# Optimization experiments

Measured on AMD Instinct MI355X. Metric: run time of the kernel, lower is better.

## Reference

```python
import jax, jax.numpy as jnp
import numpy as np

N_JOBS, N_MACH = 30, 20
N = N_JOBS * N_MACH          # 600 nodes
IN_DIM = 2
H = 128                      # hidden_dim_feature_extractor
HA = 256                     # hidden_dim_actor
HC = 256                     # hidden_dim_critic
E = 9600                     # edges
BN_EPS = 1e-5


def setup_inputs() -> dict:
    key = jax.random.key(0)
    ks = jax.random.split(key, 16)
    init = lambda k, shp: (jax.random.normal(k, shp, jnp.float32) * 0.05)
    d = {
        "features": jax.random.normal(ks[0], (N, IN_DIM), jnp.float32),
        "edge_index": jax.random.randint(ks[1], (2, E), 0, N, jnp.int32),
        # GIN layer 0 MLP: Linear(IN,H) -> BN -> ReLU -> Linear(H,H)
        "g0_W0": init(ks[2], (IN_DIM, H)), "g0_b0": jnp.zeros((H,), jnp.float32),
        "g0_gamma": jnp.ones((H,), jnp.float32), "g0_beta": jnp.zeros((H,), jnp.float32),
        "g0_W1": init(ks[3], (H, H)), "g0_b1": jnp.zeros((H,), jnp.float32),
        # GIN layer 1 MLP: Linear(H,H) -> BN -> ReLU -> Linear(H,H)
        "g1_W0": init(ks[4], (H, H)), "g1_b0": jnp.zeros((H,), jnp.float32),
        "g1_gamma": jnp.ones((H,), jnp.float32), "g1_beta": jnp.zeros((H,), jnp.float32),
        "g1_W1": init(ks[5], (H, H)), "g1_b1": jnp.zeros((H,), jnp.float32),
        # actor MLP: Linear(3H,HA) -> ReLU -> Linear(HA,1)
        "a_W0": init(ks[6], (3 * H, HA)), "a_b0": jnp.zeros((HA,), jnp.float32),
        "a_W1": init(ks[7], (HA, 1)), "a_b1": jnp.zeros((1,), jnp.float32),
        # critic MLP: Linear(H,HC) -> ReLU -> Linear(HC,1)
        "c_W0": init(ks[8], (H, HC)), "c_b0": jnp.zeros((HC,), jnp.float32),
        "c_W1": init(ks[9], (HC, 1)), "c_b1": jnp.zeros((1,), jnp.float32),
    }
    return d


def _gin_mlp(h, W0, b0, gamma, beta, W1, b1):
    # Linear -> BatchNorm(train-mode batch stats) -> ReLU -> Linear
    h1 = h @ W0 + b0
    mu = h1.mean(axis=0)
    var = h1.var(axis=0)
    h1 = gamma * (h1 - mu) * jax.lax.rsqrt(var + BN_EPS) + beta
    return jax.nn.relu(h1) @ W1 + b1


def reference(features, edge_index,
              g0_W0, g0_b0, g0_gamma, g0_beta, g0_W1, g0_b1,
              g1_W0, g1_b0, g1_gamma, g1_beta, g1_W1, g1_b1,
              a_W0, a_b0, a_W1, a_b1,
              c_W0, c_b0, c_W1, c_b1):
    src, dst = edge_index[0], edge_index[1]

    def gin(x, *mlp_params):
        # GINConv with eps=0: MLP(x + sum_{j in N(i)} x_j)
        agg = jax.ops.segment_sum(x[src], dst, num_segments=N)
        return _gin_mlp(x + agg, *mlp_params)

    h = gin(features, g0_W0, g0_b0, g0_gamma, g0_beta, g0_W1, g0_b1)
    h = gin(h, g1_W0, g1_b0, g1_gamma, g1_beta, g1_W1, g1_b1)   # (N, H)

    # graph pooling: (ones/N) @ h  == mean over nodes
    ge = h.mean(axis=0, keepdims=True)                           # (1, H)
    value = jax.nn.relu(ge @ c_W0 + c_b0) @ c_W1 + c_b1          # (1, 1)

    # s_a_pairs row k (k = i*N + j): [ge, h[j] (tile), h[i] (repeat_interleave)]
    # Fuse concat + first actor matmul by splitting a_W0 into three H-blocks.
    Ws, Wn1, Wn2 = a_W0[:H], a_W0[H:2 * H], a_W0[2 * H:]
    pre = (ge @ Ws + a_b0)[None, :, :] + (h @ Wn1)[None, :, :] + (h @ Wn2)[:, None, :]
    logits = jax.nn.relu(pre).reshape(N * N, HA) @ a_W1 + a_b1   # (N^2, 1)
    pi = jax.nn.softmax(logits, axis=0)
    return pi, value
```

## Files before the change

kernel.cpp:

```cpp
#include <hip/hip_runtime.h>
#include <math.h>

#define N_NODES 600
#define N_EDGES 9600
#define HDIM    128
#define HA      256
#define HC      256
#define NN      360000
#define BN_EPS  1e-5f
#define NTILE   361

#define OFF_U      0
#define OFF_BCONST 1200
#define OFF_BF     1456
#define OFF_SUMZ   1584
#define OFF_SUMZ2  1712
#define OFF_R1SUM  1840
#define OFF_RACC   1968
#define OFF_SUMA   2736
#define OFF_CSR    3248
#define OFF_WF     13456
#define OFF_WC1    29840
#define OFF_WC2    62608
#define OFF_WGS    95376
#define OFF_Z      128144
#define OFF_A      204944
#define OFF_B      358544

typedef _Float16 h2 __attribute__((ext_vector_type(2)));
typedef _Float16 h4 __attribute__((ext_vector_type(4)));
typedef _Float16 h8 __attribute__((ext_vector_type(8)));

__device__ __forceinline__ float dot2acc(h2 a, h2 b, float c) {
#if __has_builtin(__builtin_amdgcn_fdot2)
  return __builtin_amdgcn_fdot2(a, b, c, false);
#else
  return c + (float)a.x * (float)b.x + (float)a.y * (float)b.y;
#endif
}

__device__ __forceinline__ h2 relu2(h2 x) {
  h2 z = {(_Float16)0, (_Float16)0};
#if __has_builtin(__builtin_elementwise_max)
  return __builtin_elementwise_max(x, z);
#else
  h2 r;
  r.x = x.x > z.x ? x.x : z.x;
  r.y = x.y > z.y ? x.y : z.y;
  return r;
#endif
}

__device__ __forceinline__ h4 toh4(float4 v) {
  h4 r;
  r.x = (_Float16)v.x; r.y = (_Float16)v.y;
  r.z = (_Float16)v.z; r.w = (_Float16)v.w;
  return r;
}

struct KP {
  const float* feat; const int* ei;
  const float *g0W0, *g0ga, *g0be, *g0W1, *g0b1;
  const float *g1W0, *g1ga, *g1be, *g1W1, *g1b1;
  const float *aW0, *ab0, *aW1;
  const float *cW0, *cb0, *cW1, *cb1;
  float* ws; float* out;
};

__global__ __launch_bounds__(256) void k_indep(KP p) {
  __shared__ float sm[1536];
  const int b = blockIdx.x, t = threadIdx.x;

  if (b < 25) {
    float* us = sm;
    if (t < 48) us[t] = 0.f;
    __syncthreads();
    const int lo = b * 24, hi = lo + 24;
    for (int e = t; e < N_EDGES; e += 256) {
      int d = p.ei[N_EDGES + e];
      if (d >= lo && d < hi) {
        int s = p.ei[e];
        atomicAdd(&us[2 * (d - lo)],     p.feat[2 * s]);
        atomicAdd(&us[2 * (d - lo) + 1], p.feat[2 * s + 1]);
      }
    }
    __syncthreads();
    if (t < 48) p.ws[OFF_U + b * 48 + t] = us[t] + p.feat[b * 48 + t];
  } else if (b == 25) {
    int* si = (int*)sm;
    int* cnt = si; int* bs = si + 600; int* off = si + 856;
    int* rs_g = (int*)(p.ws + OFF_CSR);
    int* src_g = rs_g + 604;
    for (int i = t; i < 600; i += 256) cnt[i] = 0;
    __syncthreads();
    for (int e = t; e < N_EDGES; e += 256) atomicAdd(&cnt[p.ei[N_EDGES + e]], 1);
    __syncthreads();
    int lsum = 0;
    if (t < 200) lsum = cnt[3 * t] + cnt[3 * t + 1] + cnt[3 * t + 2];
    bs[t] = lsum; __syncthreads();
    for (int d = 1; d < 256; d <<= 1) {
      int v = (t >= d) ? bs[t - d] : 0;
      __syncthreads();
      bs[t] += v;
      __syncthreads();
    }
    if (t < 200) {
      int base = bs[t] - lsum;
      off[3 * t] = base;
      off[3 * t + 1] = base + cnt[3 * t];
      off[3 * t + 2] = base + cnt[3 * t] + cnt[3 * t + 1];
    }
    if (t == 0) off[600] = N_EDGES;
    __syncthreads();
    for (int i = t; i < 601; i += 256) rs_g[i] = off[i];
    for (int i = t; i < 600; i += 256) cnt[i] = off[i];
    __syncthreads();
    for (int e = t; e < N_EDGES; e += 256) {
      int d = p.ei[N_EDGES + e];
      int pos = atomicAdd(&cnt[d], 1);
      src_g[pos] = p.ei[e];
    }
  } else if (b < 42) {
    int o = (b - 26) * 1024 + t * 4;
    int j = o >> 7, c = o & 127;
    float4 acc = make_float4(0, 0, 0, 0);
#pragma unroll 8
    for (int m = 0; m < HDIM; m++) {
      float w = p.g0W1[j * HDIM + m];
      const float4 v = *(const float4*)(p.g1W0 + m * HDIM + c);
      acc.x += w * v.x; acc.y += w * v.y; acc.z += w * v.z; acc.w += w * v.w;
    }
    *(float4*)(p.ws + OFF_WF + j * HDIM + c) = acc;
  } else {
    p.ws[OFF_RACC + t] = 0.f;
    if (t < 128) {
      float a2 = 0.f;
#pragma unroll 8
      for (int m = 0; m < HDIM; m++) a2 += p.g0b1[m] * p.g1W0[m * HDIM + t];
      p.ws[OFF_BF + t] = a2;
      p.ws[OFF_SUMZ + t] = 0.f;
      p.ws[OFF_SUMZ2 + t] = 0.f;
      p.ws[OFF_R1SUM + t] = 0.f;
    }
  }
}

__global__ __launch_bounds__(256) void k_zagg(KP p) {
  __shared__ float2 u2[600];
  __shared__ float bn[384];
  __shared__ float r0agg[512];
  __shared__ float red[256];
  __shared__ float wred[24];
  const int b = blockIdx.x, t = threadIdx.x;

  if (b >= 150) {
    if (b < 246) {
      int o = (b - 150) * 1024 + t * 4;
      int mat = o >> 15, rem = o & 32767;
      int j = rem >> 8, k = rem & 255;
      int rowbase = (mat == 0) ? HDIM : (mat == 1 ? 2 * HDIM : 0);
      const float* aw = p.aW0 + rowbase * HA + k;
      float4 acc = make_float4(0, 0, 0, 0);
#pragma unroll 8
      for (int m = 0; m < HDIM; m++) {
        float w = p.g1W1[j * HDIM + m];
        const float4 v = *(const float4*)(aw + m * HA);
        acc.x += w * v.x; acc.y += w * v.y; acc.z += w * v.z; acc.w += w * v.w;
      }
      int dst = (mat == 0) ? OFF_WC1 : (mat == 1 ? OFF_WC2 : OFF_WGS);
      *(float4*)(p.ws + dst + j * HA + k) = acc;
    } else {
      float acc = 0.f;
#pragma unroll 8
      for (int m = 0; m < HDIM; m++) {
        float gb = p.g1b1[m];
        acc += gb * (p.aW0[m * HA + t] + p.aW0[(HDIM + m) * HA + t] +
                     p.aW0[(2 * HDIM + m) * HA + t]);
      }
      p.ws[OFF_BCONST + t] = p.ab0[t] + acc;
    }
    return;
  }

  const int n0 = b * 4;
  const float2* ug = (const float2*)(p.ws + OFF_U);
  for (int i = t; i < 600; i += 256) u2[i] = ug[i];
  __syncthreads();
  float s0 = 0, s1 = 0, s00 = 0, s11 = 0, s01 = 0;
  for (int n = t; n < N_NODES; n += 256) {
    float u0 = u2[n].x, u1 = u2[n].y;
    s0 += u0; s1 += u1; s00 += u0 * u0; s11 += u1 * u1; s01 += u0 * u1;
  }
#pragma unroll
  for (int off = 32; off > 0; off >>= 1) {
    s0  += __shfl_xor(s0, off);  s1  += __shfl_xor(s1, off);
    s00 += __shfl_xor(s00, off); s11 += __shfl_xor(s11, off);
    s01 += __shfl_xor(s01, off);
  }
  const int wv = t >> 6, ln = t & 63;
  if (ln == 0) {
    wred[wv * 5 + 0] = s0;  wred[wv * 5 + 1] = s1;  wred[wv * 5 + 2] = s00;
    wred[wv * 5 + 3] = s11; wred[wv * 5 + 4] = s01;
  }
  __syncthreads();
  if (t < HDIM) {
    float tot[5];
#pragma unroll
    for (int q = 0; q < 5; q++)
      tot[q] = wred[q] + wred[5 + q] + wred[10 + q] + wred[15 + q];
    float m0 = tot[0] / 600.f, m1 = tot[1] / 600.f;
    float v00 = tot[2] / 600.f - m0 * m0;
    float v11 = tot[3] / 600.f - m1 * m1;
    float v01 = tot[4] / 600.f - m0 * m1;
    float W00 = p.g0W0[t], W01 = p.g0W0[HDIM + t];
    float var = W00 * W00 * v00 + W01 * W01 * v11 + 2.f * W00 * W01 * v01;
    float sc = p.g0ga[t] * rsqrtf(var + BN_EPS);
    float mu = m0 * W00 + m1 * W01;
    bn[t] = sc * W00; bn[128 + t] = sc * W01; bn[256 + t] = p.g0be[t] - mu * sc;
  }
  __syncthreads();
  const int* rs = (const int*)(p.ws + OFF_CSR);
  const int* srcv = rs + 604;
#pragma unroll
  for (int pq = 0; pq < 2; pq++) {
    int idx = pq * 256 + t, n = idx >> 7, c = idx & 127, node = n0 + n;
    float b0c = bn[c], b1c = bn[128 + c], b2c = bn[256 + c];
    float2 uo = u2[node];
    float acc = fmaxf(uo.x * b0c + uo.y * b1c + b2c, 0.f);
    int e0 = rs[node], e1 = rs[node + 1];
    for (int e = e0; e < e1; e++) {
      float2 us = u2[srcv[e]];
      acc += fmaxf(us.x * b0c + us.y * b1c + b2c, 0.f);
    }
    r0agg[n * 128 + c] = acc;
  }
  __syncthreads();
  const float* Wf = p.ws + OFF_WF;
  const float* bf = p.ws + OFF_BF;
  float zs = 0.f, zs2 = 0.f;
#pragma unroll
  for (int pq = 0; pq < 2; pq++) {
    int idx = pq * 256 + t, n = idx >> 7, c = idx & 127, node = n0 + n;
    const float* row = r0agg + n * 128;
    int deg = rs[node + 1] - rs[node];
    float acc = (1.f + (float)deg) * bf[c];
#pragma unroll 8
    for (int j = 0; j < HDIM; j++) acc += row[j] * Wf[j * HDIM + c];
    p.ws[OFF_Z + node * HDIM + c] = acc;
    zs += acc; zs2 += acc * acc;
  }
  red[t] = zs; __syncthreads();
  if (t < 128) atomicAdd(&p.ws[OFF_SUMZ + t], red[t] + red[t + 128]);
  __syncthreads();
  red[t] = zs2; __syncthreads();
  if (t < 128) atomicAdd(&p.ws[OFF_SUMZ2 + t], red[t] + red[t + 128]);
}

__global__ __launch_bounds__(256) void k_rab(KP p) {
  __shared__ float r1[4 * 128];
  __shared__ float scl[128], shf[128], rsum4[128];
  const int b = blockIdx.x, t = threadIdx.x, n0 = b * 4;
  if (t < 128) {
    float mu = p.ws[OFF_SUMZ + t] * (1.f / 600.f);
    float var = p.ws[OFF_SUMZ2 + t] * (1.f / 600.f) - mu * mu;
    float sc = p.g1ga[t] * rsqrtf(var + BN_EPS);
    scl[t] = sc; shf[t] = p.g1be[t] - mu * sc;
  }
  __syncthreads();
#pragma unroll
  for (int pq = 0; pq < 2; pq++) {
    int idx = pq * 256 + t, n = idx >> 7, j = idx & 127;
    float z = p.ws[OFF_Z + (n0 + n) * HDIM + j];
    r1[n * 128 + j] = fmaxf(z * scl[j] + shf[j], 0.f);
  }
  __syncthreads();
  if (t < 128) {
    float s = r1[t] + r1[128 + t] + r1[256 + t] + r1[384 + t];
    rsum4[t] = s;
    atomicAdd(&p.ws[OFF_R1SUM + t], s);
  }
  __syncthreads();
  const float* wc1 = p.ws + OFF_WC1;
  const float* wc2 = p.ws + OFF_WC2;
  const float* wgs = p.ws + OFF_WGS;
  float a0 = 0, a1 = 0, a2 = 0, a3 = 0, b0 = 0, b1 = 0, b2 = 0, b3 = 0, rc = 0;
#pragma unroll 4
  for (int j = 0; j < HDIM; j++) {
    float w1 = wc1[j * HA + t], w2 = wc2[j * HA + t], wg = wgs[j * HA + t];
    float r0v = r1[j], r1v = r1[128 + j], r2v = r1[256 + j], r3v = r1[384 + j];
    a0 += r0v * w1; a1 += r1v * w1; a2 += r2v * w1; a3 += r3v * w1;
    b0 += r0v * w2; b1 += r1v * w2; b2 += r2v * w2; b3 += r3v * w2;
    rc += rsum4[j] * wg;
  }
  atomicAdd(&p.ws[OFF_RACC + t], rc);
  float* A = p.ws + OFF_A; float* Bm = p.ws + OFF_B;
  A[n0 * HA + t] = a0; A[(n0 + 1) * HA + t] = a1;
  A[(n0 + 2) * HA + t] = a2; A[(n0 + 3) * HA + t] = a3;
  Bm[n0 * HA + t] = b0; Bm[(n0 + 1) * HA + t] = b1;
  Bm[(n0 + 2) * HA + t] = b2; Bm[(n0 + 3) * HA + t] = b3;
}

__global__ __launch_bounds__(256) void k_heads(KP p) {
  __shared__ h4 AsL[2048];
  __shared__ h4 BsL[2048];
  __shared__ h4 wlp[64];
  __shared__ h4 hsp[64];
  __shared__ float hsl[256];
  __shared__ float ge[128];
  __shared__ float geh[128];
  __shared__ float red[256];
  const int b = blockIdx.x, t = threadIdx.x;

  hsl[t] = p.ws[OFF_RACC + t] * (1.f / 600.f) + p.ws[OFF_BCONST + t];

  if (b == 0) {
    if (t < 128) ge[t] = p.ws[OFF_R1SUM + t] * (1.f / 600.f);
    __syncthreads();
    if (t < 128) {
      float a0 = p.g1b1[t], a1 = 0.f, a2 = 0.f, a3 = 0.f;
#pragma unroll 4
      for (int j = 0; j < HDIM; j += 4) {
        a0 += ge[j]     * p.g1W1[(j)     * HDIM + t];
        a1 += ge[j + 1] * p.g1W1[(j + 1) * HDIM + t];
        a2 += ge[j + 2] * p.g1W1[(j + 2) * HDIM + t];
        a3 += ge[j + 3] * p.g1W1[(j + 3) * HDIM + t];
      }
      geh[t] = (a0 + a1) + (a2 + a3);
    }
    __syncthreads();
    {
      float v0 = p.cb0[t], v1 = 0.f, v2 = 0.f, v3 = 0.f;
#pragma unroll 4
      for (int c = 0; c < HDIM; c += 4) {
        v0 += geh[c]     * p.cW0[(c)     * HC + t];
        v1 += geh[c + 1] * p.cW0[(c + 1) * HC + t];
        v2 += geh[c + 2] * p.cW0[(c + 2) * HC + t];
        v3 += geh[c + 3] * p.cW0[(c + 3) * HC + t];
      }
      float v = fmaxf((v0 + v1) + (v2 + v3), 0.f);
      red[t] = v * p.cW1[t];
    }
    __syncthreads();
    for (int off = 128; off > 0; off >>= 1) {
      if (t < off) red[t] += red[t + off];
      __syncthreads();
    }
    if (t == 0) p.out[NN] = red[0] + p.cb1[0];
  }
  __syncthreads();
  if (t < 64) {
    wlp[t] = toh4(*(const float4*)(p.aW1 + 4 * t));
    hsp[t] = toh4(*(const float4*)(hsl + 4 * t));
  }
  __syncthreads();

  const int tj = b % 19, ti = b / 19;
  const int j0 = tj * 32, i0 = ti * 32;
  const float* A  = p.ws + OFF_A;
  const float* Bm = p.ws + OFF_B;
#pragma unroll
  for (int q = 0; q < 8; q++) {
    int f = q * 256 + t;
    int r = f >> 6;
    int c4 = f & 63;
    int k = c4 * 4;
    int sw = c4 * 32 + (r ^ (c4 & 30));
    float4 av = (j0 + r < N_NODES) ? *(const float4*)(A + (j0 + r) * HA + k)
                                   : make_float4(0, 0, 0, 0);
    AsL[sw] = toh4(av) + hsp[c4];
    float4 bv = (i0 + r < N_NODES) ? *(const float4*)(Bm + (i0 + r) * HA + k)
                                   : make_float4(0, 0, 0, 0);
    BsL[sw] = toh4(bv);
  }
  __syncthreads();

  const int tx = t & 15, ty = t >> 4;
  const int jl = tx * 2, il = ty * 2;
  float a00 = 0, a01 = 0, a10 = 0, a11 = 0;
#pragma unroll 8
  for (int kk2 = 0; kk2 < 64; kk2++) {
    int s = kk2 & 30;
    h8 va = *(h8*)&AsL[kk2 * 32 + (jl ^ s)];
    h8 vb = *(h8*)&BsL[kk2 * 32 + (il ^ s)];
    h4 vw = wlp[kk2];
    h2 wlo = __builtin_shufflevector(vw, vw, 0, 1);
    h2 whi = __builtin_shufflevector(vw, vw, 2, 3);
    h2 aj0lo = __builtin_shufflevector(va, va, 0, 1);
    h2 aj0hi = __builtin_shufflevector(va, va, 2, 3);
    h2 aj1lo = __builtin_shufflevector(va, va, 4, 5);
    h2 aj1hi = __builtin_shufflevector(va, va, 6, 7);
    h2 bi0lo = __builtin_shufflevector(vb, vb, 0, 1);
    h2 bi0hi = __builtin_shufflevector(vb, vb, 2, 3);
    h2 bi1lo = __builtin_shufflevector(vb, vb, 4, 5);
    h2 bi1hi = __builtin_shufflevector(vb, vb, 6, 7);
    a00 = dot2acc(relu2(aj0lo + bi0lo), wlo, a00);
    a00 = dot2acc(relu2(aj0hi + bi0hi), whi, a00);
    a01 = dot2acc(relu2(aj1lo + bi0lo), wlo, a01);
    a01 = dot2acc(relu2(aj1hi + bi0hi), whi, a01);
    a10 = dot2acc(relu2(aj0lo + bi1lo), wlo, a10);
    a10 = dot2acc(relu2(aj0hi + bi1hi), whi, a10);
    a11 = dot2acc(relu2(aj1lo + bi1lo), wlo, a11);
    a11 = dot2acc(relu2(aj1hi + bi1hi), whi, a11);
  }

  const int gi = i0 + il, gj = j0 + jl;
  const bool vi0 = gi < N_NODES, vi1 = gi + 1 < N_NODES;
  const bool vj0 = gj < N_NODES, vj1 = gj + 1 < N_NODES;
  float s = 0.f;
  if (vi0 && vj0) { float e = __expf(a00); p.out[gi * N_NODES + gj] = e; s += e; }
  if (vi0 && vj1) { float e = __expf(a01); p.out[gi * N_NODES + gj + 1] = e; s += e; }
  if (vi1 && vj0) { float e = __expf(a10); p.out[(gi + 1) * N_NODES + gj] = e; s += e; }
  if (vi1 && vj1) { float e = __expf(a11); p.out[(gi + 1) * N_NODES + gj + 1] = e; s += e; }
  __syncthreads();
  red[t] = s;
  __syncthreads();
  for (int off = 128; off > 0; off >>= 1) {
    if (t < off) red[t] += red[t + off];
    __syncthreads();
  }
  if (t == 0) p.ws[OFF_SUMA + b] = red[0];
}

__global__ __launch_bounds__(256) void k_fin(KP p) {
  __shared__ float red[256];
  const int b = blockIdx.x, t = threadIdx.x;
  const float* suma = p.ws + OFF_SUMA;
  float s = (t < NTILE ? suma[t] : 0.f) + (t + 256 < NTILE ? suma[t + 256] : 0.f);
  red[t] = s;
  __syncthreads();
  for (int off = 128; off > 0; off >>= 1) {
    if (t < off) red[t] += red[t + off];
    __syncthreads();
  }
  const float inv = 1.0f / red[0];
#pragma unroll
  for (int pass = 0; pass < 3; pass++) {
    int f4 = pass * 256 + t;
    if (f4 < 600) {
      int r = f4 / 150, c4 = (f4 % 150) * 4;
      float* pp = p.out + (b * 4 + r) * N_NODES + c4;
      float4 v = *(const float4*)pp;
      v.x *= inv; v.y *= inv; v.z *= inv; v.w *= inv;
      *(float4*)pp = v;
    }
  }
}

extern "C" void kernel_launch(void* const* d_in, const int* in_sizes, int n_in,
                              void* d_out, int out_size, void* d_ws, size_t ws_size,
                              hipStream_t stream) {
  KP p;
  p.feat = (const float*)d_in[0];
  p.ei   = (const int*)  d_in[1];
  p.g0W0 = (const float*)d_in[2];
  p.g0ga = (const float*)d_in[4];  p.g0be = (const float*)d_in[5];
  p.g0W1 = (const float*)d_in[6];  p.g0b1 = (const float*)d_in[7];
  p.g1W0 = (const float*)d_in[8];
  p.g1ga = (const float*)d_in[10]; p.g1be = (const float*)d_in[11];
  p.g1W1 = (const float*)d_in[12]; p.g1b1 = (const float*)d_in[13];
  p.aW0  = (const float*)d_in[14]; p.ab0  = (const float*)d_in[15];
  p.aW1  = (const float*)d_in[16];
  p.cW0  = (const float*)d_in[18]; p.cb0  = (const float*)d_in[19];
  p.cW1  = (const float*)d_in[20]; p.cb1  = (const float*)d_in[21];
  p.ws   = (float*)d_ws;
  p.out  = (float*)d_out;

  k_indep<<<43,    256, 0, stream>>>(p);
  k_zagg <<<247,   256, 0, stream>>>(p);
  k_rab  <<<150,   256, 0, stream>>>(p);
  k_heads<<<NTILE, 256, 0, stream>>>(p);
  k_fin  <<<150,   256, 0, stream>>>(p);
}
```

Baseline: 78.41 us.

## Fuse five kernels into one persistent megakernel with atomic-counter stage gating

Replaces the five back-to-back kernel launches with a single kernel whose blocks are partitioned by stage. Blocks wait on global atomic arrival counters before consuming the previous stage's results, and a memset zeroes the counters and accumulators. The aim is to remove per-launch overhead and let independent precompute overlap with dependent stages. It relies on block dispatch order to avoid deadlock, since later-stage blocks spin while occupying CUs; all 951 blocks fit only if enough are resident, and the spin has a timeout break that could silently corrupt results.

After: 263.2 us. 236% more time.

```diff
diff --git a/kernel.cpp b/kernel.cpp
--- a/kernel.cpp
+++ b/kernel.cpp
@@ -10,22 +10,39 @@
 #define BN_EPS  1e-5f
 #define NTILE   361
 
-#define OFF_U      0
-#define OFF_BCONST 1200
-#define OFF_BF     1456
-#define OFF_SUMZ   1584
-#define OFF_SUMZ2  1712
-#define OFF_R1SUM  1840
-#define OFF_RACC   1968
-#define OFF_SUMA   2736
-#define OFF_CSR    3248
-#define OFF_WF     13456
-#define OFF_WC1    29840
-#define OFF_WC2    62608
-#define OFF_WGS    95376
-#define OFF_Z      128144
-#define OFF_A      204944
-#define OFF_B      358544
+#define B_PRE0   0
+#define B_CSR    25
+#define B_WF0    26
+#define B_BF     42
+#define B_WC0    43
+#define B_ZAGG0  140
+#define B_RAB0   290
+#define B_HEAD0  440
+#define B_FIN0   801
+#define NBLKS    951
+#define C1_TGT   43
+#define C2_TGT   247
+#define C3_TGT   150
+#define C4_TGT   361
+
+#define OFF_CNT    0
+#define OFF_SUMZ   16
+#define OFF_SUMZ2  144
+#define OFF_R1SUM  272
+#define OFF_RACC   400
+#define ZERO_BYTES (656 * 4)
+#define OFF_U      656
+#define OFF_BCONST 1856
+#define OFF_BF     2112
+#define OFF_SUMA   2240
+#define OFF_CSR    2608
+#define OFF_WF     12816
+#define OFF_WC1    29200
+#define OFF_WC2    61968
+#define OFF_WGS    94736
+#define OFF_Z      127504
+#define OFF_A      204304
+#define OFF_B      357904
 
 typedef _Float16 h2 __attribute__((ext_vector_type(2)));
 typedef _Float16 h4 __attribute__((ext_vector_type(4)));
@@ -67,12 +84,31 @@
   float* ws; float* out;
 };
 
-__global__ __launch_bounds__(256) void k_indep(KP p) {
-  __shared__ float sm[1536];
+__device__ __forceinline__ void gate(int* c, int target) {
+  if (threadIdx.x == 0) {
+    int it = 0;
+    while (__hip_atomic_load(c, __ATOMIC_RELAXED, __HIP_MEMORY_SCOPE_AGENT) < target) {
+      __builtin_amdgcn_s_sleep(1);
+      if (++it > (1 << 26)) break;
+    }
+  }
+  __syncthreads();
+  __threadfence();
+}
+__device__ __forceinline__ void arrive(int* c) {
+  __syncthreads();
+  __threadfence();
+  if (threadIdx.x == 0)
+    __hip_atomic_fetch_add(c, 1, __ATOMIC_RELEASE, __HIP_MEMORY_SCOPE_AGENT);
+}
+
+__global__ __launch_bounds__(256, 4) void mega(KP p) {
+  __shared__ float smem[9216];
   const int b = blockIdx.x, t = threadIdx.x;
-
-  if (b < 25) {
-    float* us = sm;
+  int* cnt = (int*)(p.ws + OFF_CNT);
+
+  if (b < B_CSR) {
+    float* us = smem;
     if (t < 48) us[t] = 0.f;
     __syncthreads();
     const int lo = b * 24, hi = lo + 24;
@@ -86,17 +122,18 @@
     }
     __syncthreads();
     if (t < 48) p.ws[OFF_U + b * 48 + t] = us[t] + p.feat[b * 48 + t];
-  } else if (b == 25) {
-    int* si = (int*)sm;
-    int* cnt = si; int* bs = si + 600; int* off = si + 856;
+    arrive(&cnt[0]);
+  } else if (b == B_CSR) {
+    int* si = (int*)smem;
+    int* cn = si; int* bs = si + 600; int* off = si + 856;
     int* rs_g = (int*)(p.ws + OFF_CSR);
     int* src_g = rs_g + 604;
-    for (int i = t; i < 600; i += 256) cnt[i] = 0;
-    __syncthreads();
-    for (int e = t; e < N_EDGES; e += 256) atomicAdd(&cnt[p.ei[N_EDGES + e]], 1);
+    for (int i = t; i < 600; i += 256) cn[i] = 0;
+    __syncthreads();
+    for (int e = t; e < N_EDGES; e += 256) atomicAdd(&cn[p.ei[N_EDGES + e]], 1);
     __syncthreads();
     int lsum = 0;
-    if (t < 200) lsum = cnt[3 * t] + cnt[3 * t + 1] + cnt[3 * t + 2];
+    if (t < 200) lsum = cn[3 * t] + cn[3 * t + 1] + cn[3 * t + 2];
     bs[t] = lsum; __syncthreads();
     for (int d = 1; d < 256; d <<= 1) {
       int v = (t >= d) ? bs[t - d] : 0;
@@ -107,21 +144,22 @@
     if (t < 200) {
       int base = bs[t] - lsum;
       off[3 * t] = base;
-      off[3 * t + 1] = base + cnt[3 * t];
-      off[3 * t + 2] = base + cnt[3 * t] + cnt[3 * t + 1];
+      off[3 * t + 1] = base + cn[3 * t];
+      off[3 * t + 2] = base + cn[3 * t] + cn[3 * t + 1];
     }
     if (t == 0) off[600] = N_EDGES;
     __syncthreads();
     for (int i = t; i < 601; i += 256) rs_g[i] = off[i];
-    for (int i = t; i < 600; i += 256) cnt[i] = off[i];
+    for (int i = t; i < 600; i += 256) cn[i] = off[i];
     __syncthreads();
     for (int e = t; e < N_EDGES; e += 256) {
       int d = p.ei[N_EDGES + e];
-      int pos = atomicAdd(&cnt[d], 1);
+      int pos = atomicAdd(&cn[d], 1);
       src_g[pos] = p.ei[e];
     }
-  } else if (b < 42) {
-    int o = (b - 26) * 1024 + t * 4;
+    arrive(&cnt[0]);
+  } else if (b < B_BF) {
+    int o = (b - B_WF0) * 1024 + t * 4;
     int j = o >> 7, c = o & 127;
     float4 acc = make_float4(0, 0, 0, 0);
 #pragma unroll 8
@@ -131,31 +169,19 @@
       acc.x += w * v.x; acc.y += w * v.y; acc.z += w * v.z; acc.w += w * v.w;
     }
     *(float4*)(p.ws + OFF_WF + j * HDIM + c) = acc;
-  } else {
-    p.ws[OFF_RACC + t] = 0.f;
+    arrive(&cnt[0]);
+  } else if (b == B_BF) {
     if (t < 128) {
       float a2 = 0.f;
 #pragma unroll 8
       for (int m = 0; m < HDIM; m++) a2 += p.g0b1[m] * p.g1W0[m * HDIM + t];
       p.ws[OFF_BF + t] = a2;
-      p.ws[OFF_SUMZ + t] = 0.f;
-      p.ws[OFF_SUMZ2 + t] = 0.f;
-      p.ws[OFF_R1SUM + t] = 0.f;
-    }
-  }
-}
-
-__global__ __launch_bounds__(256) void k_zagg(KP p) {
-  __shared__ float2 u2[600];
-  __shared__ float bn[384];
-  __shared__ float r0agg[512];
-  __shared__ float red[256];
-  __shared__ float wred[24];
-  const int b = blockIdx.x, t = threadIdx.x;
-
-  if (b >= 150) {
-    if (b < 246) {
-      int o = (b - 150) * 1024 + t * 4;
+    }
+    arrive(&cnt[0]);
+  } else if (b < B_ZAGG0) {
+    int idx = b - B_WC0;
+    if (idx < 96) {
+      int o = idx * 1024 + t * 4;
       int mat = o >> 15, rem = o & 32767;
       int j = rem >> 8, k = rem & 255;
       int rowbase = (mat == 0) ? HDIM : (mat == 1 ? 2 * HDIM : 0);
@@ -179,269 +205,275 @@
       }
       p.ws[OFF_BCONST + t] = p.ab0[t] + acc;
     }
-    return;
-  }
-
-  const int n0 = b * 4;
-  const float2* ug = (const float2*)(p.ws + OFF_U);
-  for (int i = t; i < 600; i += 256) u2[i] = ug[i];
-  __syncthreads();
-  float s0 = 0, s1 = 0, s00 = 0, s11 = 0, s01 = 0;
-  for (int n = t; n < N_NODES; n += 256) {
-    float u0 = u2[n].x, u1 = u2[n].y;
-    s0 += u0; s1 += u1; s00 += u0 * u0; s11 += u1 * u1; s01 += u0 * u1;
-  }
-#pragma unroll
-  for (int off = 32; off > 0; off >>= 1) {
-    s0  += __shfl_xor(s0, off);  s1  += __shfl_xor(s1, off);
-    s00 += __shfl_xor(s00, off); s11 += __shfl_xor(s11, off);
-    s01 += __shfl_xor(s01, off);
-  }
-  const int wv = t >> 6, ln = t & 63;
-  if (ln == 0) {
-    wred[wv * 5 + 0] = s0;  wred[wv * 5 + 1] = s1;  wred[wv * 5 + 2] = s00;
-    wred[wv * 5 + 3] = s11; wred[wv * 5 + 4] = s01;
-  }
-  __syncthreads();
-  if (t < HDIM) {
-    float tot[5];
-#pragma unroll
-    for (int q = 0; q < 5; q++)
-      tot[q] = wred[q] + wred[5 + q] + wred[10 + q] + wred[15 + q];
-    float m0 = tot[0] / 600.f, m1 = tot[1] / 600.f;
-    float v00 = tot[2] / 600.f - m0 * m0;
-    float v11 = tot[3] / 600.f - m1 * m1;
-    float v01 = tot[4] / 600.f - m0 * m1;
-    float W00 = p.g0W0[t], W01 = p.g0W0[HDIM + t];
-    float var = W00 * W00 * v00 + W01 * W01 * v11 + 2.f * W00 * W01 * v01;
-    float sc = p.g0ga[t] * rsqrtf(var + BN_EPS);
-    float mu = m0 * W00 + m1 * W01;
-    bn[t] = sc * W00; bn[128 + t] = sc * W01; bn[256 + t] = p.g0be[t] - mu * sc;
-  }
-  __syncthreads();
-  const int* rs = (const int*)(p.ws + OFF_CSR);
-  const int* srcv = rs + 604;
-#pragma unroll
-  for (int pq = 0; pq < 2; pq++) {
-    int idx = pq * 256 + t, n = idx >> 7, c = idx & 127, node = n0 + n;
-    float b0c = bn[c], b1c = bn[128 + c], b2c = bn[256 + c];
-    float2 uo = u2[node];
-    float acc = fmaxf(uo.x * b0c + uo.y * b1c + b2c, 0.f);
-    int e0 = rs[node], e1 = rs[node + 1];
-    for (int e = e0; e < e1; e++) {
-      float2 us = u2[srcv[e]];
-      acc += fmaxf(us.x * b0c + us.y * b1c + b2c, 0.f);
-    }
-    r0agg[n * 128 + c] = acc;
-  }
-  __syncthreads();
-  const float* Wf = p.ws + OFF_WF;
-  const float* bf = p.ws + OFF_BF;
-  float zs = 0.f, zs2 = 0.f;
-#pragma unroll
-  for (int pq = 0; pq < 2; pq++) {
-    int idx = pq * 256 + t, n = idx >> 7, c = idx & 127, node = n0 + n;
-    const float* row = r0agg + n * 128;
-    int deg = rs[node + 1] - rs[node];
-    float acc = (1.f + (float)deg) * bf[c];
+    arrive(&cnt[1]);
+  } else if (b < B_RAB0) {
+    gate(&cnt[0], C1_TGT);
+    float2* u2   = (float2*)smem;
+    float* bn    = smem + 1200;
+    float* r0agg = smem + 1584;
+    float* red   = smem + 2096;
+    float* wred  = smem + 2352;
+    const int n0 = (b - B_ZAGG0) * 4;
+    const float2* ug = (const float2*)(p.ws + OFF_U);
+    for (int i = t; i < 600; i += 256) u2[i] = ug[i];
+    __syncthreads();
+    float s0 = 0, s1 = 0, s00 = 0, s11 = 0, s01 = 0;
+    for (int n = t; n < N_NODES; n += 256) {
+      float u0 = u2[n].x, u1 = u2[n].y;
+      s0 += u0; s1 += u1; s00 += u0 * u0; s11 += u1 * u1; s01 += u0 * u1;
+    }
+#pragma unroll
+    for (int off = 32; off > 0; off >>= 1) {
+      s0  += __shfl_xor(s0, off);  s1  += __shfl_xor(s1, off);
+      s00 += __shfl_xor(s00, off); s11 += __shfl_xor(s11, off);
+      s01 += __shfl_xor(s01, off);
+    }
+    const int wv = t >> 6, ln = t & 63;
+    if (ln == 0) {
+      wred[wv * 5 + 0] = s0;  wred[wv * 5 + 1] = s1;  wred[wv * 5 + 2] = s00;
+      wred[wv * 5 + 3] = s11; wred[wv * 5 + 4] = s01;
+    }
+    __syncthreads();
+    if (t < HDIM) {
+      float tot[5];
+#pragma unroll
+      for (int q = 0; q < 5; q++)
+        tot[q] = wred[q] + wred[5 + q] + wred[10 + q] + wred[15 + q];
+      float m0 = tot[0] / 600.f, m1 = tot[1] / 600.f;
+      float v00 = tot[2] / 600.f - m0 * m0;
+      float v11 = tot[3] / 600.f - m1 * m1;
+      float v01 = tot[4] / 600.f - m0 * m1;
+      float W00 = p.g0W0[t], W01 = p.g0W0[HDIM + t];
+      float var = W00 * W00 * v00 + W01 * W01 * v11 + 2.f * W00 * W01 * v01;
+      float sc = p.g0ga[t] * rsqrtf(var + BN_EPS);
+      float mu = m0 * W00 + m1 * W01;
+      bn[t] = sc * W00; bn[128 + t] = sc * W01; bn[256 + t] = p.g0be[t] - mu * sc;
+    }
+    __syncthreads();
+    const int* rs = (const int*)(p.ws + OFF_CSR);
+    const int* srcv = rs + 604;
+#pragma unroll
+    for (int pq = 0; pq < 2; pq++) {
+      int idx = pq * 256 + t, n = idx >> 7, c = idx & 127, node = n0 + n;
+      float b0c = bn[c], b1c = bn[128 + c], b2c = bn[256 + c];
+      float2 uo = u2[node];
+      float acc = fmaxf(uo.x * b0c + uo.y * b1c + b2c, 0.f);
+      int e0 = rs[node], e1 = rs[node + 1];
+      for (int e = e0; e < e1; e++) {
+        float2 us = u2[srcv[e]];
+        acc += fmaxf(us.x * b0c + us.y * b1c + b2c, 0.f);
+      }
+      r0agg[n * 128 + c] = acc;
+    }
+    __syncthreads();
+    const float* Wf = p.ws + OFF_WF;
+    const float* bf = p.ws + OFF_BF;
+    float zs = 0.f, zs2 = 0.f;
+#pragma unroll
+    for (int pq = 0; pq < 2; pq++) {
+      int idx = pq * 256 + t, n = idx >> 7, c = idx & 127, node = n0 + n;
+      const float* row = r0agg + n * 128;
+      int deg = rs[node + 1] - rs[node];
+      float acc = (1.f + (float)deg) * bf[c];
 #pragma unroll 8
-    for (int j = 0; j < HDIM; j++) acc += row[j] * Wf[j * HDIM + c];
-    p.ws[OFF_Z + node * HDIM + c] = acc;
-    zs += acc; zs2 += acc * acc;
-  }
-  red[t] = zs; __syncthreads();
-  if (t < 128) atomicAdd(&p.ws[OFF_SUMZ + t], red[t] + red[t + 128]);
-  __syncthreads();
-  red[t] = zs2; __syncthreads();
-  if (t < 128) atomicAdd(&p.ws[OFF_SUMZ2 + t], red[t] + red[t + 128]);
-}
-
-__global__ __launch_bounds__(256) void k_rab(KP p) {
-  __shared__ float r1[4 * 128];
-  __shared__ float scl[128], shf[128], rsum4[128];
-  const int b = blockIdx.x, t = threadIdx.x, n0 = b * 4;
-  if (t < 128) {
-    float mu = p.ws[OFF_SUMZ + t] * (1.f / 600.f);
-    float var = p.ws[OFF_SUMZ2 + t] * (1.f / 600.f) - mu * mu;
-    float sc = p.g1ga[t] * rsqrtf(var + BN_EPS);
-    scl[t] = sc; shf[t] = p.g1be[t] - mu * sc;
-  }
-  __syncthreads();
-#pragma unroll
-  for (int pq = 0; pq < 2; pq++) {
-    int idx = pq * 256 + t, n = idx >> 7, j = idx & 127;
-    float z = p.ws[OFF_Z + (n0 + n) * HDIM + j];
-    r1[n * 128 + j] = fmaxf(z * scl[j] + shf[j], 0.f);
-  }
-  __syncthreads();
-  if (t < 128) {
-    float s = r1[t] + r1[128 + t] + r1[256 + t] + r1[384 + t];
-    rsum4[t] = s;
-    atomicAdd(&p.ws[OFF_R1SUM + t], s);
-  }
-  __syncthreads();
-  const float* wc1 = p.ws + OFF_WC1;
-  const float* wc2 = p.ws + OFF_WC2;
-  const float* wgs = p.ws + OFF_WGS;
-  float a0 = 0, a1 = 0, a2 = 0, a3 = 0, b0 = 0, b1 = 0, b2 = 0, b3 = 0, rc = 0;
+      for (int j = 0; j < HDIM; j++) acc += row[j] * Wf[j * HDIM + c];
+      p.ws[OFF_Z + node * HDIM + c] = acc;
+      zs += acc; zs2 += acc * acc;
+    }
+    red[t] = zs; __syncthreads();
+    if (t < 128) atomicAdd(&p.ws[OFF_SUMZ + t], red[t] + red[t + 128]);
+    __syncthreads();
+    red[t] = zs2; __syncthreads();
+    if (t < 128) atomicAdd(&p.ws[OFF_SUMZ2 + t], red[t] + red[t + 128]);
+    arrive(&cnt[1]);
+  } else if (b < B_HEAD0) {
+    gate(&cnt[1], C2_TGT);
+    float* r1    = smem;
+    float* scl   = smem + 512;
+    float* shf   = smem + 640;
+    float* rsum4 = smem + 768;
+    const int n0 = (b - B_RAB0) * 4;
+    if (t < 128) {
+      float mu = p.ws[OFF_SUMZ + t] * (1.f / 600.f);
+      float var = p.ws[OFF_SUMZ2 + t] * (1.f / 600.f) - mu * mu;
+      float sc = p.g1ga[t] * rsqrtf(var + BN_EPS);
+      scl[t] = sc; shf[t] = p.g1be[t] - mu * sc;
+    }
+    __syncthreads();
+#pragma unroll
+    for (int pq = 0; pq < 2; pq++) {
+      int idx = pq * 256 + t, n = idx >> 7, j = idx & 127;
+      float z = p.ws[OFF_Z + (n0 + n) * HDIM + j];
+      r1[n * 128 + j] = fmaxf(z * scl[j] + shf[j], 0.f);
+    }
+    __syncthreads();
+    if (t < 128) {
+      float s = r1[t] + r1[128 + t] + r1[256 + t] + r1[384 + t];
+      rsum4[t] = s;
+      atomicAdd(&p.ws[OFF_R1SUM + t], s);
+    }
+    __syncthreads();
+    const float* wc1 = p.ws + OFF_WC1;
+    const float* wc2 = p.ws + OFF_WC2;
+    const float* wgs = p.ws + OFF_WGS;
+    float a0 = 0, a1 = 0, a2 = 0, a3 = 0, b0 = 0, b1 = 0, b2 = 0, b3 = 0, rc = 0;
 #pragma unroll 4
-  for (int j = 0; j < HDIM; j++) {
-    float w1 = wc1[j * HA + t], w2 = wc2[j * HA + t], wg = wgs[j * HA + t];
-    float r0v = r1[j], r1v = r1[128 + j], r2v = r1[256 + j], r3v = r1[384 + j];
-    a0 += r0v * w1; a1 += r1v * w1; a2 += r2v * w1; a3 += r3v * w1;
-    b0 += r0v * w2; b1 += r1v * w2; b2 += r2v * w2; b3 += r3v * w2;
-    rc += rsum4[j] * wg;
-  }
-  atomicAdd(&p.ws[OFF_RACC + t], rc);
-  float* A = p.ws + OFF_A; float* Bm = p.ws + OFF_B;
-  A[n0 * HA + t] = a0; A[(n0 + 1) * HA + t] = a1;
-  A[(n0 + 2) * HA + t] = a2; A[(n0 + 3) * HA + t] = a3;
-  Bm[n0 * HA + t] = b0; Bm[(n0 + 1) * HA + t] = b1;
-  Bm[(n0 + 2) * HA + t] = b2; Bm[(n0 + 3) * HA + t] = b3;
-}
-
-__global__ __launch_bounds__(256) void k_heads(KP p) {
-  __shared__ h4 AsL[2048];
-  __shared__ h4 BsL[2048];
-  __shared__ h4 wlp[64];
-  __shared__ h4 hsp[64];
-  __shared__ float hsl[256];
-  __shared__ float ge[128];
-  __shared__ float geh[128];
-  __shared__ float red[256];
-  const int b = blockIdx.x, t = threadIdx.x;
-
-  hsl[t] = p.ws[OFF_RACC + t] * (1.f / 600.f) + p.ws[OFF_BCONST + t];
-
-  if (b == 0) {
-    if (t < 128) ge[t] = p.ws[OFF_R1SUM + t] * (1.f / 600.f);
-    __syncthreads();
-    if (t < 128) {
-      float a0 = p.g1b1[t], a1 = 0.f, a2 = 0.f, a3 = 0.f;
+    for (int j = 0; j < HDIM; j++) {
+      float w1 = wc1[j * HA + t], w2 = wc2[j * HA + t], wg = wgs[j * HA + t];
+      float r0v = r1[j], r1v = r1[128 + j], r2v = r1[256 + j], r3v = r1[384 + j];
+      a0 += r0v * w1; a1 += r1v * w1; a2 += r2v * w1; a3 += r3v * w1;
+      b0 += r0v * w2; b1 += r1v * w2; b2 += r2v * w2; b3 += r3v * w2;
+      rc += rsum4[j] * wg;
+    }
+    atomicAdd(&p.ws[OFF_RACC + t], rc);
+    float* A = p.ws + OFF_A; float* Bm = p.ws + OFF_B;
+    A[n0 * HA + t] = a0; A[(n0 + 1) * HA + t] = a1;
+    A[(n0 + 2) * HA + t] = a2; A[(n0 + 3) * HA + t] = a3;
+    Bm[n0 * HA + t] = b0; Bm[(n0 + 1) * HA + t] = b1;
+    Bm[(n0 + 2) * HA + t] = b2; Bm[(n0 + 3) * HA + t] = b3;
+    arrive(&cnt[2]);
+  } else if (b < B_FIN0) {
+    gate(&cnt[2], C3_TGT);
+    h4* AsL    = (h4*)smem;
+    h4* BsL    = (h4*)(smem + 4096);
+    h4* wlp    = (h4*)(smem + 8192);
+    h4* hsp    = (h4*)(smem + 8320);
+    float* hsl = smem + 8448;
+    float* ge  = smem + 8704;
+    float* geh = smem + 8832;
+    float* red = smem + 8960;
+    const int hb = b - B_HEAD0;
+
+    hsl[t] = p.ws[OFF_RACC + t] * (1.f / 600.f) + p.ws[OFF_BCONST + t];
+
+    if (hb == 0) {
+      if (t < 128) ge[t] = p.ws[OFF_R1SUM + t] * (1.f / 600.f);
+      __syncthreads();
+      if (t < 128) {
+        float a0 = p.g1b1[t], a1 = 0.f, a2 = 0.f, a3 = 0.f;
 #pragma unroll 4
-      for (int j = 0; j < HDIM; j += 4) {
-        a0 += ge[j]     * p.g1W1[(j)     * HDIM + t];
-        a1 += ge[j + 1] * p.g1W1[(j + 1) * HDIM + t];
-        a2 += ge[j + 2] * p.g1W1[(j + 2) * HDIM + t];
-        a3 += ge[j + 3] * p.g1W1[(j + 3) * HDIM + t];
-      }
-      geh[t] = (a0 + a1) + (a2 + a3);
-    }
-    __syncthreads();
-    {
-      float v0 = p.cb0[t], v1 = 0.f, v2 = 0.f, v3 = 0.f;
+        for (int j = 0; j < HDIM; j += 4) {
+          a0 += ge[j]     * p.g1W1[(j)     * HDIM + t];
+          a1 += ge[j + 1] * p.g1W1[(j + 1) * HDIM + t];
+          a2 += ge[j + 2] * p.g1W1[(j + 2) * HDIM + t];
+          a3 += ge[j + 3] * p.g1W1[(j + 3) * HDIM + t];
+        }
+        geh[t] = (a0 + a1) + (a2 + a3);
+      }
+      __syncthreads();
+      {
+        float v0 = p.cb0[t], v1 = 0.f, v2 = 0.f, v3 = 0.f;
 #pragma unroll 4
-      for (int c = 0; c < HDIM; c += 4) {
-        v0 += geh[c]     * p.cW0[(c)     * HC + t];
-        v1 += geh[c + 1] * p.cW0[(c + 1) * HC + t];
-        v2 += geh[c + 2] * p.cW0[(c + 2) * HC + t];
-        v3 += geh[c + 3] * p.cW0[(c + 3) * HC + t];
-      }
-      float v = fmaxf((v0 + v1) + (v2 + v3), 0.f);
-      red[t] = v * p.cW1[t];
-    }
+        for (int c = 0; c < HDIM; c += 4) {
+          v0 += geh[c]     * p.cW0[(c)     * HC + t];
+          v1 += geh[c + 1] * p.cW0[(c + 1) * HC + t];
+          v2 += geh[c + 2] * p.cW0[(c + 2) * HC + t];
+          v3 += geh[c + 3] * p.cW0[(c + 3) * HC + t];
+        }
+        float v = fmaxf((v0 + v1) + (v2 + v3), 0.f);
+        red[t] = v * p.cW1[t];
+      }
+      __syncthreads();
+      for (int off = 128; off > 0; off >>= 1) {
+        if (t < off) red[t] += red[t + off];
+        __syncthreads();
+      }
+      if (t == 0) p.out[NN] = red[0] + p.cb1[0];
+    }
+    __syncthreads();
+    if (t < 64) {
+      wlp[t] = toh4(*(const float4*)(p.aW1 + 4 * t));
+      hsp[t] = toh4(*(const float4*)(hsl + 4 * t));
+    }
+    __syncthreads();
+
+    const int tj = hb % 19, ti = hb / 19;
+    const int j0 = tj * 32, i0 = ti * 32;
+    const float* A  = p.ws + OFF_A;
+    const float* Bm = p.ws + OFF_B;
+#pragma unroll
+    for (int q = 0; q < 8; q++) {
+      int f = q * 256 + t;
+      int r = f >> 6, c4 = f & 63, k = c4 * 4;
+      int sw = c4 * 32 + (r ^ (c4 & 30));
+      float4 av = (j0 + r < N_NODES) ? *(const float4*)(A + (j0 + r) * HA + k)
+                                     : make_float4(0, 0, 0, 0);
+      AsL[sw] = toh4(av) + hsp[c4];
+      float4 bv = (i0 + r < N_NODES) ? *(const float4*)(Bm + (i0 + r) * HA + k)
+                                     : make_float4(0, 0, 0, 0);
+      BsL[sw] = toh4(bv);
+    }
+    __syncthreads();
+
+    const int tx = t & 15, ty = t >> 4;
+    const int jl = tx * 2, il = ty * 2;
+    float a00 = 0, a01 = 0, a10 = 0, a11 = 0;
+#pragma unroll 8
+    for (int kk2 = 0; kk2 < 64; kk2++) {
+      int s = kk2 & 30;
+      h8 va = *(h8*)&AsL[kk2 * 32 + (jl ^ s)];
+      h8 vb = *(h8*)&BsL[kk2 * 32 + (il ^ s)];
+      h4 vw = wlp[kk2];
+      h2 wlo = __builtin_shufflevector(vw, vw, 0, 1);
+      h2 whi = __builtin_shufflevector(vw, vw, 2, 3);
+      h2 aj0lo = __builtin_shufflevector(va, va, 0, 1);
+      h2 aj0hi = __builtin_shufflevector(va, va, 2, 3);
+      h2 aj1lo = __builtin_shufflevector(va, va, 4, 5);
+      h2 aj1hi = __builtin_shufflevector(va, va, 6, 7);
+      h2 bi0lo = __builtin_shufflevector(vb, vb, 0, 1);
+      h2 bi0hi = __builtin_shufflevector(vb, vb, 2, 3);
+      h2 bi1lo = __builtin_shufflevector(vb, vb, 4, 5);
+      h2 bi1hi = __builtin_shufflevector(vb, vb, 6, 7);
+      a00 = dot2acc(relu2(aj0lo + bi0lo), wlo, a00);
+      a00 = dot2acc(relu2(aj0hi + bi0hi), whi, a00);
+      a01 = dot2acc(relu2(aj1lo + bi0lo), wlo, a01);
+      a01 = dot2acc(relu2(aj1hi + bi0hi), whi, a01);
+      a10 = dot2acc(relu2(aj0lo + bi1lo), wlo, a10);
+      a10 = dot2acc(relu2(aj0hi + bi1hi), whi, a10);
+      a11 = dot2acc(relu2(aj1lo + bi1lo), wlo, a11);
+      a11 = dot2acc(relu2(aj1hi + bi1hi), whi, a11);
+    }
+
+    const int gi = i0 + il, gj = j0 + jl;
+    const bool vi0 = gi < N_NODES, vi1 = gi + 1 < N_NODES;
+    const bool vj0 = gj < N_NODES, vj1 = gj + 1 < N_NODES;
+    float s = 0.f;
+    if (vi0 && vj0) { float e = __expf(a00); p.out[gi * N_NODES + gj] = e; s += e; }
+    if (vi0 && vj1) { float e = __expf(a01); p.out[gi * N_NODES + gj + 1] = e; s += e; }
+    if (vi1 && vj0) { float e = __expf(a10); p.out[(gi + 1) * N_NODES + gj] = e; s += e; }
+    if (vi1 && vj1) { float e = __expf(a11); p.out[(gi + 1) * N_NODES + gj + 1] = e; s += e; }
+    __syncthreads();
+    red[t] = s;
     __syncthreads();
     for (int off = 128; off > 0; off >>= 1) {
       if (t < off) red[t] += red[t + off];
       __syncthreads();
     }
-    if (t == 0) p.out[NN] = red[0] + p.cb1[0];
-  }
-  __syncthreads();
-  if (t < 64) {
-    wlp[t] = toh4(*(const float4*)(p.aW1 + 4 * t));
-    hsp[t] = toh4(*(const float4*)(hsl + 4 * t));
-  }
-  __syncthreads();
-
-  const int tj = b % 19, ti = b / 19;
-  const int j0 = tj * 32, i0 = ti * 32;
-  const float* A  = p.ws + OFF_A;
-  const float* Bm = p.ws + OFF_B;
-#pragma unroll
-  for (int q = 0; q < 8; q++) {
-    int f = q * 256 + t;
-    int r = f >> 6;
-    int c4 = f & 63;
-    int k = c4 * 4;
-    int sw = c4 * 32 + (r ^ (c4 & 30));
-    float4 av = (j0 + r < N_NODES) ? *(const float4*)(A + (j0 + r) * HA + k)
-                                   : make_float4(0, 0, 0, 0);
-    AsL[sw] = toh4(av) + hsp[c4];
-    float4 bv = (i0 + r < N_NODES) ? *(const float4*)(Bm + (i0 + r) * HA + k)
-                                   : make_float4(0, 0, 0, 0);
-    BsL[sw] = toh4(bv);
-  }
-  __syncthreads();
-
-  const int tx = t & 15, ty = t >> 4;
-  const int jl = tx * 2, il = ty * 2;
-  float a00 = 0, a01 = 0, a10 = 0, a11 = 0;
-#pragma unroll 8
-  for (int kk2 = 0; kk2 < 64; kk2++) {
-    int s = kk2 & 30;
-    h8 va = *(h8*)&AsL[kk2 * 32 + (jl ^ s)];
-    h8 vb = *(h8*)&BsL[kk2 * 32 + (il ^ s)];
-    h4 vw = wlp[kk2];
-    h2 wlo = __builtin_shufflevector(vw, vw, 0, 1);
-    h2 whi = __builtin_shufflevector(vw, vw, 2, 3);
-    h2 aj0lo = __builtin_shufflevector(va, va, 0, 1);
-    h2 aj0hi = __builtin_shufflevector(va, va, 2, 3);
-    h2 aj1lo = __builtin_shufflevector(va, va, 4, 5);
-    h2 aj1hi = __builtin_shufflevector(va, va, 6, 7);
-    h2 bi0lo = __builtin_shufflevector(vb, vb, 0, 1);
-    h2 bi0hi = __builtin_shufflevector(vb, vb, 2, 3);
-    h2 bi1lo = __builtin_shufflevector(vb, vb, 4, 5);
-    h2 bi1hi = __builtin_shufflevector(vb, vb, 6, 7);
-    a00 = dot2acc(relu2(aj0lo + bi0lo), wlo, a00);
-    a00 = dot2acc(relu2(aj0hi + bi0hi), whi, a00);
-    a01 = dot2acc(relu2(aj1lo + bi0lo), wlo, a01);
-    a01 = dot2acc(relu2(aj1hi + bi0hi), whi, a01);
-    a10 = dot2acc(relu2(aj0lo + bi1lo), wlo, a10);
-    a10 = dot2acc(relu2(aj0hi + bi1hi), whi, a10);
-    a11 = dot2acc(relu2(aj1lo + bi1lo), wlo, a11);
-    a11 = dot2acc(relu2(aj1hi + bi1hi), whi, a11);
-  }
-
-  const int gi = i0 + il, gj = j0 + jl;
-  const bool vi0 = gi < N_NODES, vi1 = gi + 1 < N_NODES;
-  const bool vj0 = gj < N_NODES, vj1 = gj + 1 < N_NODES;
-  float s = 0.f;
-  if (vi0 && vj0) { float e = __expf(a00); p.out[gi * N_NODES + gj] = e; s += e; }
-  if (vi0 && vj1) { float e = __expf(a01); p.out[gi * N_NODES + gj + 1] = e; s += e; }
-  if (vi1 && vj0) { float e = __expf(a10); p.out[(gi + 1) * N_NODES + gj] = e; s += e; }
-  if (vi1 && vj1) { float e = __expf(a11); p.out[(gi + 1) * N_NODES + gj + 1] = e; s += e; }
-  __syncthreads();
-  red[t] = s;
-  __syncthreads();
-  for (int off = 128; off > 0; off >>= 1) {
-    if (t < off) red[t] += red[t + off];
-    __syncthreads();
-  }
-  if (t == 0) p.ws[OFF_SUMA + b] = red[0];
-}
-
-__global__ __launch_bounds__(256) void k_fin(KP p) {
-  __shared__ float red[256];
-  const int b = blockIdx.x, t = threadIdx.x;
-  const float* suma = p.ws + OFF_SUMA;
-  float s = (t < NTILE ? suma[t] : 0.f) + (t + 256 < NTILE ? suma[t + 256] : 0.f);
-  red[t] = s;
-  __syncthreads();
-  for (int off = 128; off > 0; off >>= 1) {
-    if (t < off) red[t] += red[t + off];
-    __syncthreads();
-  }
-  const float inv = 1.0f / red[0];
-#pragma unroll
-  for (int pass = 0; pass < 3; pass++) {
-    int f4 = pass * 256 + t;
-    if (f4 < 600) {
-      int r = f4 / 150, c4 = (f4 % 150) * 4;
-      float* pp = p.out + (b * 4 + r) * N_NODES + c4;
-      float4 v = *(const float4*)pp;
-      v.x *= inv; v.y *= inv; v.z *= inv; v.w *= inv;
-      *(float4*)pp = v;
+    if (t == 0) p.ws[OFF_SUMA + hb] = red[0];
+    arrive(&cnt[3]);
+  } else {
+    gate(&cnt[3], C4_TGT);
+    float* red = smem;
+    const int fb = b - B_FIN0;
+    const float* suma = p.ws + OFF_SUMA;
+    float s = (t < NTILE ? suma[t] : 0.f) + (t + 256 < NTILE ? suma[t + 256] : 0.f);
+    red[t] = s;
+    __syncthreads();
+    for (int off = 128; off > 0; off >>= 1) {
+      if (t < off) red[t] += red[t + off];
+      __syncthreads();
+    }
+    const float inv = 1.0f / red[0];
+#pragma unroll
+    for (int pass = 0; pass < 3; pass++) {
+      int f4 = pass * 256 + t;
+      if (f4 < 600) {
+        int r = f4 / 150, c4 = (f4 % 150) * 4;
+        float* pp = p.out + (fb * 4 + r) * N_NODES + c4;
+        float4 v = *(const float4*)pp;
+        v.x *= inv; v.y *= inv; v.z *= inv; v.w *= inv;
+        *(float4*)pp = v;
+      }
     }
   }
 }
@@ -465,9 +497,6 @@
   p.ws   = (float*)d_ws;
   p.out  = (float*)d_out;
 
-  k_indep<<<43,    256, 0, stream>>>(p);
-  k_zagg <<<247,   256, 0, stream>>>(p);
-  k_rab  <<<150,   256, 0, stream>>>(p);
-  k_heads<<<NTILE, 256, 0, stream>>>(p);
-  k_fin  <<<150,   256, 0, stream>>>(p);
-}
+  hipMemsetAsync(p.ws, 0, ZERO_BYTES, stream);
+  mega<<<NBLKS, 256, 0, stream>>>(p);
+}
```
